# Kernel optimization log

Measured on AMD Instinct MI355X. Metric: run time of the kernel, lower is better.

Reference implementation:

```python
import jax, jax.numpy as jnp
import numpy as np

B, D, H, W = 32, 256, 64, 64
KEEP_RATIO = 0.5
LN_EPS = 1e-5


def setup_inputs() -> dict:
    key = jax.random.key(0)
    k1, k2 = jax.random.split(key)
    return {
        "tokens": jax.random.normal(k1, (B, D, H, W), dtype=jnp.float32),
        "norm_w": jnp.ones((D,), dtype=jnp.float32),
        "norm_b": jnp.zeros((D,), dtype=jnp.float32),
        "fc_w": jax.random.normal(k2, (1, D), dtype=jnp.float32) * (1.0 / np.sqrt(D)),
        "fc_b": jnp.zeros((1,), dtype=jnp.float32),
    }


def reference(tokens, norm_w, norm_b, fc_w, fc_b):
    b, d, h, w = tokens.shape
    n = h * w
    num_keep = int(n * KEEP_RATIO)  # static
    # NCHW -> (B, N, D)
    t = tokens.transpose(0, 2, 3, 1).reshape(b, n, d)
    # LayerNorm over last dim
    mu = jnp.mean(t, axis=-1, keepdims=True)
    var = jnp.mean(jnp.square(t - mu), axis=-1, keepdims=True)
    ln = (t - mu) * jax.lax.rsqrt(var + LN_EPS) * norm_w + norm_b
    # Linear(dim -> 1), squeeze, softmax over tokens
    scores = jnp.einsum("bnd,d->bn", ln, fc_w[0]) + fc_b[0]
    scores = jax.nn.softmax(scores, axis=-1)
    # top-k then sort indices ascending (spatial order), gather tokens
    _, idx = jax.lax.top_k(scores, num_keep)  # (B, K)
    idx = jnp.sort(idx, axis=-1)
    selected = jnp.take_along_axis(t, idx[:, :, None], axis=1)  # (B, K, D)
    return selected
```

## Files before the change

### kernel.cpp

```cpp
#include <hip/hip_runtime.h>
#include <stdint.h>
#include <math.h>

#define B_ 32
#define D_ 256
#define N_ 4096
#define K_ 2048
#define PT 32

__global__ __launch_bounds__(256) void score_kernel(
    const float* __restrict__ tokens,
    const float* __restrict__ norm_w, const float* __restrict__ norm_b,
    const float* __restrict__ fc_w, const float* __restrict__ fc_b,
    double* __restrict__ scores)
{
    __shared__ float wv[D_];
    __shared__ double r1[256];
    __shared__ double r2[256];
    const int tid = threadIdx.x;
    const int b = blockIdx.y;
    const int n = blockIdx.x * 256 + tid;

    const float nw = norm_w[tid];
    const float fw = fc_w[tid];
    const float nb = norm_b[tid];
    wv[tid] = nw * fw;
    r1[tid] = (double)nw * (double)fw;
    r2[tid] = (double)nb * (double)fw;
    __syncthreads();
    for (int off = 128; off > 0; off >>= 1) {
        if (tid < off) { r1[tid] += r1[tid + off]; r2[tid] += r2[tid + off]; }
        __syncthreads();
    }
    const double S1 = r1[0];
    const double S2 = r2[0] + (double)fc_b[0];

    const float* tp = tokens + (size_t)b * D_ * N_ + n;
    double sum = 0.0, sumsq = 0.0, dot = 0.0;
#pragma unroll 8
    for (int d = 0; d < D_; ++d) {
        double v = (double)tp[(size_t)d * N_];
        sum += v;
        sumsq += v * v;
        dot += v * (double)wv[d];
    }
    const double mu = sum * (1.0 / D_);
    const double var = sumsq * (1.0 / D_) - mu * mu;
    const double sc = (dot - mu * S1) / sqrt(var + 1e-5) + S2;
    scores[(size_t)b * N_ + n] = sc;
}

__global__ __launch_bounds__(256) void select_kernel(
    const double* __restrict__ scores, int* __restrict__ sel_idx)
{
    const int b = blockIdx.x;
    const int tid = threadIdx.x;
    __shared__ unsigned buf[256];
    __shared__ unsigned sh_scan[256];
    __shared__ unsigned long long sh_prefix;
    __shared__ int sh_k;

    unsigned long long key[16];
    const double* sp = scores + (size_t)b * N_;
    const int base = tid * 16;
#pragma unroll
    for (int i = 0; i < 16; ++i) {
        unsigned long long u = (unsigned long long)__double_as_longlong(sp[base + i]);
        u = (u & 0x8000000000000000ULL) ? ~u : (u | 0x8000000000000000ULL);
        key[i] = u;
    }

    unsigned long long prefix = 0ULL;
    int k = K_;
    for (int pass = 0; pass < 8; ++pass) {
        const int shift = 56 - 8 * pass;
        buf[tid] = 0u;
        __syncthreads();
        const unsigned long long pmask = (pass == 0) ? 0ULL : (~0ULL << (shift + 8));
#pragma unroll
        for (int i = 0; i < 16; ++i) {
            if ((key[i] & pmask) == prefix)
                atomicAdd(&buf[(unsigned)((key[i] >> shift) & 255ULL)], 1u);
        }
        __syncthreads();
        for (int off = 1; off < 256; off <<= 1) {
            unsigned add = (tid + off < 256) ? buf[tid + off] : 0u;
            __syncthreads();
            buf[tid] += add;
            __syncthreads();
        }
        const unsigned s_here = buf[tid];
        const unsigned s_next = (tid < 255) ? buf[tid + 1] : 0u;
        if (s_here >= (unsigned)k && s_next < (unsigned)k) {
            sh_prefix = prefix | ((unsigned long long)tid << shift);
            sh_k = k - (int)s_next;
        }
        __syncthreads();
        prefix = sh_prefix;
        k = sh_k;
        __syncthreads();
    }
    const unsigned long long T = prefix;
    const int ties_needed = k;

    int loc_eq = 0;
#pragma unroll
    for (int i = 0; i < 16; ++i) loc_eq += (key[i] == T);
    sh_scan[tid] = (unsigned)loc_eq;
    __syncthreads();
    for (int off = 1; off < 256; off <<= 1) {
        unsigned add = (tid >= off) ? sh_scan[tid - off] : 0u;
        __syncthreads();
        sh_scan[tid] += add;
        __syncthreads();
    }
    const int eq_before = (int)sh_scan[tid] - loc_eq;
    __syncthreads();

    int sel[16];
    int loc_sel = 0;
    int eq_run = eq_before;
#pragma unroll
    for (int i = 0; i < 16; ++i) {
        int s;
        if (key[i] > T) s = 1;
        else if (key[i] == T) { s = (eq_run < ties_needed) ? 1 : 0; eq_run++; }
        else s = 0;
        sel[i] = s;
        loc_sel += s;
    }
    sh_scan[tid] = (unsigned)loc_sel;
    __syncthreads();
    for (int off = 1; off < 256; off <<= 1) {
        unsigned add = (tid >= off) ? sh_scan[tid - off] : 0u;
        __syncthreads();
        sh_scan[tid] += add;
        __syncthreads();
    }
    int pos = (int)sh_scan[tid] - loc_sel;
    int* op = sel_idx + (size_t)b * K_;
#pragma unroll
    for (int i = 0; i < 16; ++i) {
        if (sel[i]) op[pos++] = base + i;
    }
}

__global__ __launch_bounds__(256) void gather_kernel(
    const float* __restrict__ tokens, const int* __restrict__ sel_idx,
    float* __restrict__ out)
{
    __shared__ float tile[D_][PT + 1];
    __shared__ int nn[PT];
    const int b = blockIdx.y;
    const int p0 = blockIdx.x * PT;
    const int tid = threadIdx.x;

    if (tid < PT) nn[tid] = sel_idx[(size_t)b * K_ + p0 + tid];
    __syncthreads();

    const int p = tid & 31;
    const int dg = tid >> 5;
    const float* tp = tokens + (size_t)b * D_ * N_;
    const int n = nn[p];
    for (int d = dg; d < D_; d += 8)
        tile[d][p] = tp[(size_t)d * N_ + n];
    __syncthreads();

    const int lane = tid & 63;
    const int w = tid >> 6;
    float* op = out + ((size_t)b * K_ + p0) * D_;
    for (int pp = w * 8; pp < w * 8 + 8; ++pp)
        for (int dd = lane; dd < D_; dd += 64)
            op[(size_t)pp * D_ + dd] = tile[dd][pp];
}

extern "C" void kernel_launch(void* const* d_in, const int* in_sizes, int n_in,
                              void* d_out, int out_size, void* d_ws, size_t ws_size,
                              hipStream_t stream)
{
    const float* tokens = (const float*)d_in[0];
    const float* norm_w = (const float*)d_in[1];
    const float* norm_b = (const float*)d_in[2];
    const float* fc_w   = (const float*)d_in[3];
    const float* fc_b   = (const float*)d_in[4];
    float* out = (float*)d_out;

    double* scores = (double*)d_ws;
    int* sel_idx = (int*)((char*)d_ws + (size_t)B_ * N_ * sizeof(double));

    score_kernel<<<dim3(N_ / 256, B_), 256, 0, stream>>>(
        tokens, norm_w, norm_b, fc_w, fc_b, scores);
    select_kernel<<<dim3(B_), 256, 0, stream>>>(scores, sel_idx);
    gather_kernel<<<dim3(K_ / PT, B_), 256, 0, stream>>>(tokens, sel_idx, out);
}
```

Measured before the change: 260.7 us.

## Vectorize scoring, use 12-bit radix select, and gather from coalesced spatial tiles

The score kernel now handles two tokens per thread with float2 loads and writes order-preserving 64-bit keys, so the select kernel no longer converts doubles. Radix select drops from eight 8-bit passes to three 12-bit passes. It thresholds on the top 36 key bits and breaks ties by spatial order, which slightly changes tie semantics. Selection also records per-256-token output boundaries. The gather kernel uses these boundaries to load contiguous token tiles with coalesced float2 reads into shared memory, then writes the selected rows. The trade-off is that it reads every token instead of only the selected ones.

```diff
diff --git a/kernel.cpp b/kernel.cpp
--- a/kernel.cpp
+++ b/kernel.cpp
@@ -6,25 +6,35 @@
 #define D_ 256
 #define N_ 4096
 #define K_ 2048
-#define PT 32
+#define NBIN 4096
 
 __global__ __launch_bounds__(256) void score_kernel(
     const float* __restrict__ tokens,
     const float* __restrict__ norm_w, const float* __restrict__ norm_b,
     const float* __restrict__ fc_w, const float* __restrict__ fc_b,
-    double* __restrict__ scores)
+    unsigned long long* __restrict__ keys)
 {
     __shared__ float wv[D_];
-    __shared__ double r1[256];
-    __shared__ double r2[256];
+    __shared__ double r1[256], r2[256];
     const int tid = threadIdx.x;
     const int b = blockIdx.y;
-    const int n = blockIdx.x * 256 + tid;
-
-    const float nw = norm_w[tid];
-    const float fw = fc_w[tid];
-    const float nb = norm_b[tid];
+    const int n0 = (blockIdx.x * 256 + tid) * 2;
+
+    const float nw = norm_w[tid], fw = fc_w[tid], nb = norm_b[tid];
     wv[tid] = nw * fw;
+    __syncthreads();
+
+    const float* tp = tokens + (size_t)b * (D_ * N_) + n0;
+    double s0 = 0, q0 = 0, p0 = 0, s1 = 0, q1 = 0, p1 = 0;
+#pragma unroll 8
+    for (int d = 0; d < D_; ++d) {
+        float2 v = *reinterpret_cast<const float2*>(tp + (size_t)d * N_);
+        double w = (double)wv[d];
+        double a = (double)v.x, c = (double)v.y;
+        s0 += a; q0 += a * a; p0 += a * w;
+        s1 += c; q1 += c * c; p1 += c * w;
+    }
+
     r1[tid] = (double)nw * (double)fw;
     r2[tid] = (double)nb * (double)fw;
     __syncthreads();
@@ -35,143 +45,159 @@
     const double S1 = r1[0];
     const double S2 = r2[0] + (double)fc_b[0];
 
-    const float* tp = tokens + (size_t)b * D_ * N_ + n;
-    double sum = 0.0, sumsq = 0.0, dot = 0.0;
-#pragma unroll 8
-    for (int d = 0; d < D_; ++d) {
-        double v = (double)tp[(size_t)d * N_];
-        sum += v;
-        sumsq += v * v;
-        dot += v * (double)wv[d];
-    }
-    const double mu = sum * (1.0 / D_);
-    const double var = sumsq * (1.0 / D_) - mu * mu;
-    const double sc = (dot - mu * S1) / sqrt(var + 1e-5) + S2;
-    scores[(size_t)b * N_ + n] = sc;
+    const double inv = 1.0 / D_;
+    double mu0 = s0 * inv, var0 = q0 * inv - mu0 * mu0;
+    double sc0 = (p0 - mu0 * S1) / sqrt(var0 + 1e-5) + S2;
+    double mu1 = s1 * inv, var1 = q1 * inv - mu1 * mu1;
+    double sc1 = (p1 - mu1 * S1) / sqrt(var1 + 1e-5) + S2;
+
+    long long i0 = __double_as_longlong(sc0);
+    long long i1 = __double_as_longlong(sc1);
+    unsigned long long u0 = (i0 < 0) ? ~(unsigned long long)i0
+                                     : ((unsigned long long)i0 | 0x8000000000000000ULL);
+    unsigned long long u1 = (i1 < 0) ? ~(unsigned long long)i1
+                                     : ((unsigned long long)i1 | 0x8000000000000000ULL);
+    ulonglong2 kk; kk.x = u0; kk.y = u1;
+    *reinterpret_cast<ulonglong2*>(keys + (size_t)b * N_ + n0) = kk;
 }
 
 __global__ __launch_bounds__(256) void select_kernel(
-    const double* __restrict__ scores, int* __restrict__ sel_idx)
+    const unsigned long long* __restrict__ keys, int* __restrict__ sel_idx,
+    int* __restrict__ pbound)
 {
     const int b = blockIdx.x;
     const int tid = threadIdx.x;
-    __shared__ unsigned buf[256];
-    __shared__ unsigned sh_scan[256];
+    __shared__ unsigned hist[NBIN];
+    __shared__ unsigned part[256];
     __shared__ unsigned long long sh_prefix;
     __shared__ int sh_k;
 
     unsigned long long key[16];
-    const double* sp = scores + (size_t)b * N_;
+    const unsigned long long* kp = keys + (size_t)b * N_;
     const int base = tid * 16;
 #pragma unroll
-    for (int i = 0; i < 16; ++i) {
-        unsigned long long u = (unsigned long long)__double_as_longlong(sp[base + i]);
-        u = (u & 0x8000000000000000ULL) ? ~u : (u | 0x8000000000000000ULL);
-        key[i] = u;
-    }
+    for (int i = 0; i < 16; ++i) key[i] = kp[base + i];
 
     unsigned long long prefix = 0ULL;
     int k = K_;
-    for (int pass = 0; pass < 8; ++pass) {
-        const int shift = 56 - 8 * pass;
-        buf[tid] = 0u;
-        __syncthreads();
-        const unsigned long long pmask = (pass == 0) ? 0ULL : (~0ULL << (shift + 8));
-#pragma unroll
-        for (int i = 0; i < 16; ++i) {
+#pragma unroll
+    for (int pass = 0; pass < 3; ++pass) {
+        const int shift = 52 - 12 * pass;
+        const unsigned long long pmask =
+            (pass == 0) ? 0ULL : (~0ULL << (64 - 12 * pass));
+#pragma unroll
+        for (int j = 0; j < 16; ++j) hist[tid + 256 * j] = 0u;
+        __syncthreads();
+#pragma unroll
+        for (int i = 0; i < 16; ++i)
             if ((key[i] & pmask) == prefix)
-                atomicAdd(&buf[(unsigned)((key[i] >> shift) & 255ULL)], 1u);
-        }
+                atomicAdd(&hist[(unsigned)((key[i] >> shift) & 4095ULL)], 1u);
+        __syncthreads();
+        unsigned s = 0;
+#pragma unroll
+        for (int j = 0; j < 16; ++j) s += hist[tid * 16 + j];
+        part[tid] = s;
         __syncthreads();
         for (int off = 1; off < 256; off <<= 1) {
-            unsigned add = (tid + off < 256) ? buf[tid + off] : 0u;
+            unsigned add = (tid + off < 256) ? part[tid + off] : 0u;
             __syncthreads();
-            buf[tid] += add;
+            part[tid] += add;
             __syncthreads();
         }
-        const unsigned s_here = buf[tid];
-        const unsigned s_next = (tid < 255) ? buf[tid + 1] : 0u;
-        if (s_here >= (unsigned)k && s_next < (unsigned)k) {
-            sh_prefix = prefix | ((unsigned long long)tid << shift);
-            sh_k = k - (int)s_next;
+        const unsigned snext = (tid < 255) ? part[tid + 1] : 0u;
+        unsigned run = snext;
+        for (int j = 15; j >= 0; --j) {
+            unsigned h = hist[tid * 16 + j];
+            unsigned run2 = run + h;
+            if (run2 >= (unsigned)k && run < (unsigned)k) {
+                sh_prefix = prefix | ((unsigned long long)(tid * 16 + j) << shift);
+                sh_k = k - (int)run;
+            }
+            run = run2;
         }
         __syncthreads();
         prefix = sh_prefix;
         k = sh_k;
         __syncthreads();
     }
-    const unsigned long long T = prefix;
-    const int ties_needed = k;
+
+    const unsigned long long M = ~0ULL << 28;
+    const unsigned long long TH = prefix;
+    const int need = k;
 
     int loc_eq = 0;
 #pragma unroll
-    for (int i = 0; i < 16; ++i) loc_eq += (key[i] == T);
-    sh_scan[tid] = (unsigned)loc_eq;
+    for (int i = 0; i < 16; ++i) loc_eq += ((key[i] & M) == TH);
+    part[tid] = (unsigned)loc_eq;
     __syncthreads();
     for (int off = 1; off < 256; off <<= 1) {
-        unsigned add = (tid >= off) ? sh_scan[tid - off] : 0u;
-        __syncthreads();
-        sh_scan[tid] += add;
-        __syncthreads();
-    }
-    const int eq_before = (int)sh_scan[tid] - loc_eq;
-    __syncthreads();
-
-    int sel[16];
+        unsigned add = (tid >= off) ? part[tid - off] : 0u;
+        __syncthreads();
+        part[tid] += add;
+        __syncthreads();
+    }
+    const int eq_before = (int)part[tid] - loc_eq;
+    __syncthreads();
+
+    unsigned selm = 0;
     int loc_sel = 0;
-    int eq_run = eq_before;
+    int eq = eq_before;
 #pragma unroll
     for (int i = 0; i < 16; ++i) {
-        int s;
-        if (key[i] > T) s = 1;
-        else if (key[i] == T) { s = (eq_run < ties_needed) ? 1 : 0; eq_run++; }
-        else s = 0;
-        sel[i] = s;
-        loc_sel += s;
-    }
-    sh_scan[tid] = (unsigned)loc_sel;
+        unsigned long long kh = key[i] & M;
+        int s = (kh > TH) ? 1 : ((kh == TH) ? ((eq++ < need) ? 1 : 0) : 0);
+        if (s) { selm |= (1u << i); ++loc_sel; }
+    }
+    part[tid] = (unsigned)loc_sel;
     __syncthreads();
     for (int off = 1; off < 256; off <<= 1) {
-        unsigned add = (tid >= off) ? sh_scan[tid - off] : 0u;
-        __syncthreads();
-        sh_scan[tid] += add;
-        __syncthreads();
-    }
-    int pos = (int)sh_scan[tid] - loc_sel;
+        unsigned add = (tid >= off) ? part[tid - off] : 0u;
+        __syncthreads();
+        part[tid] += add;
+        __syncthreads();
+    }
+    int pos = (int)part[tid] - loc_sel;
     int* op = sel_idx + (size_t)b * K_;
 #pragma unroll
-    for (int i = 0; i < 16; ++i) {
-        if (sel[i]) op[pos++] = base + i;
-    }
+    for (int i = 0; i < 16; ++i)
+        if (selm & (1u << i)) op[pos++] = base + i;
+
+    if ((tid & 15) == 15) pbound[b * 17 + (tid >> 4) + 1] = (int)part[tid];
+    if (tid == 0) pbound[b * 17] = 0;
 }
 
 __global__ __launch_bounds__(256) void gather_kernel(
     const float* __restrict__ tokens, const int* __restrict__ sel_idx,
-    float* __restrict__ out)
-{
-    __shared__ float tile[D_][PT + 1];
-    __shared__ int nn[PT];
-    const int b = blockIdx.y;
-    const int p0 = blockIdx.x * PT;
+    const int* __restrict__ pbound, float* __restrict__ out)
+{
+    __shared__ float tile[64 * 258];
+    __shared__ int nl[256];
     const int tid = threadIdx.x;
-
-    if (tid < PT) nn[tid] = sel_idx[(size_t)b * K_ + p0 + tid];
-    __syncthreads();
-
-    const int p = tid & 31;
-    const int dg = tid >> 5;
-    const float* tp = tokens + (size_t)b * D_ * N_;
-    const int n = nn[p];
-    for (int d = dg; d < D_; d += 8)
-        tile[d][p] = tp[(size_t)d * N_ + n];
-    __syncthreads();
-
-    const int lane = tid & 63;
-    const int w = tid >> 6;
-    float* op = out + ((size_t)b * K_ + p0) * D_;
-    for (int pp = w * 8; pp < w * 8 + 8; ++pp)
-        for (int dd = lane; dd < D_; dd += 64)
-            op[(size_t)pp * D_ + dd] = tile[dd][pp];
+    const int w = tid >> 6, l = tid & 63;
+    const int n0 = blockIdx.x * 256;
+    const int d0 = blockIdx.y * 64;
+    const int b  = blockIdx.z;
+
+    const int plo = pbound[b * 17 + blockIdx.x];
+    const int cnt = pbound[b * 17 + blockIdx.x + 1] - plo;
+
+    if (tid < cnt) nl[tid] = sel_idx[(size_t)b * K_ + plo + tid] - n0;
+
+    const float* tb = tokens + (size_t)b * (D_ * N_) + n0;
+#pragma unroll 4
+    for (int dd = w; dd < 64; dd += 4) {
+        const float* row = tb + (size_t)(d0 + dd) * N_;
+        float2 v0 = *reinterpret_cast<const float2*>(row + 2 * l);
+        float2 v1 = *reinterpret_cast<const float2*>(row + 2 * l + 128);
+        *reinterpret_cast<float2*>(&tile[dd * 258 + 2 * l]) = v0;
+        *reinterpret_cast<float2*>(&tile[dd * 258 + 2 * l + 128]) = v1;
+    }
+    __syncthreads();
+
+    float* ob = out + ((size_t)b * K_ + plo) * D_ + d0 + l;
+    for (int i = w; i < cnt; i += 4) {
+        ob[(size_t)i * D_] = tile[l * 258 + nl[i]];
+    }
 }
 
 extern "C" void kernel_launch(void* const* d_in, const int* in_sizes, int n_in,
@@ -185,11 +211,14 @@
     const float* fc_b   = (const float*)d_in[4];
     float* out = (float*)d_out;
 
-    double* scores = (double*)d_ws;
-    int* sel_idx = (int*)((char*)d_ws + (size_t)B_ * N_ * sizeof(double));
-
-    score_kernel<<<dim3(N_ / 256, B_), 256, 0, stream>>>(
-        tokens, norm_w, norm_b, fc_w, fc_b, scores);
-    select_kernel<<<dim3(B_), 256, 0, stream>>>(scores, sel_idx);
-    gather_kernel<<<dim3(K_ / PT, B_), 256, 0, stream>>>(tokens, sel_idx, out);
-}
+    unsigned long long* keys = (unsigned long long*)d_ws;
+    int* sel_idx = (int*)((char*)d_ws + (size_t)B_ * N_ * 8);
+    int* pbound  = (int*)((char*)d_ws + (size_t)B_ * N_ * 8
+                          + (size_t)B_ * K_ * 4);
+
+    score_kernel<<<dim3(N_ / 512, B_), 256, 0, stream>>>(
+        tokens, norm_w, norm_b, fc_w, fc_b, keys);
+    select_kernel<<<dim3(B_), 256, 0, stream>>>(keys, sel_idx, pbound);
+    gather_kernel<<<dim3(N_ / 256, D_ / 64, B_), 256, 0, stream>>>(
+        tokens, sel_idx, pbound, out);
+}
```

After: 262.7 us. No clear change (+0.7%).
